# Kernel tuning notes

Measured on AMD Instinct MI355X. Metric: run time of the kernel, lower is better.

The kernel has to match this reference:

```python
import jax, jax.numpy as jnp
import numpy as np

B = 16
H_DIM = 512
N_HEADS = 8
HEAD_DIM = H_DIM // N_HEADS  # 64
EPS = 1e-5
DST_LENS = 256 + 16 * np.arange(B)  # ragged dst sizes, total 6016
SRC_LENS = 512 - 8 * np.arange(B)   # ragged src sizes, total 7232


def _pad_info(lens):
    # gather/scatter indices to move between flat ragged layout and [B, Lmax, D]
    lens = np.asarray(lens)
    off = np.concatenate([[0], np.cumsum(lens)[:-1]])
    gid = np.repeat(np.arange(len(lens)), lens)
    pos = np.arange(int(lens.sum())) - np.repeat(off, lens)
    Lmax = int(lens.max())
    mask = jnp.asarray(np.arange(Lmax)[None, :] < lens[:, None])
    return gid, pos, Lmax, mask


def _bn(x, g, b):
    # BatchNorm1d forward with batch statistics (training-mode normalization)
    m = x.mean(0)
    v = ((x - m) ** 2).mean(0)
    return (x - m) / jnp.sqrt(v + EPS) * g + b


def setup_inputs() -> dict:
    key = jax.random.key(0)
    ks = jax.random.split(key, 20)
    total_src = int(SRC_LENS.sum())
    total_dst = int(DST_LENS.sum())
    w = lambda k, shape: jax.random.normal(k, shape, jnp.float32) * 0.02
    return {
        "src_h": jax.random.normal(ks[0], (total_src, H_DIM), jnp.float32),
        "dst_h": jax.random.normal(ks[1], (total_dst, H_DIM), jnp.float32),
        "src_num_verts": jnp.asarray(SRC_LENS, jnp.int32),
        "dst_num_verts": jnp.asarray(DST_LENS, jnp.int32),
        "Wq": w(ks[2], (H_DIM, H_DIM)), "bq": w(ks[3], (H_DIM,)),
        "Wk": w(ks[4], (H_DIM, H_DIM)), "bk": w(ks[5], (H_DIM,)),
        "Wv": w(ks[6], (H_DIM, H_DIM)), "bv": w(ks[7], (H_DIM,)),
        "Wm": w(ks[8], (H_DIM, H_DIM)), "bm": w(ks[9], (H_DIM,)),
        "W1": w(ks[10], (H_DIM, 2 * H_DIM)), "b1": w(ks[11], (H_DIM,)),
        "g1": jnp.ones((H_DIM,), jnp.float32), "be1": jnp.zeros((H_DIM,), jnp.float32),
        "W2": w(ks[12], (H_DIM, H_DIM)), "b2": w(ks[13], (H_DIM,)),
        "g2": jnp.ones((H_DIM,), jnp.float32), "be2": jnp.zeros((H_DIM,), jnp.float32),
    }


def reference(src_h, dst_h, src_num_verts, dst_num_verts,
              Wq, bq, Wk, bk, Wv, bv, Wm, bm,
              W1, b1, g1, be1, W2, b2, g2, be2):
    s_lens = np.asarray(src_num_verts)
    d_lens = np.asarray(dst_num_verts)
    sg, sp, Ls, smask = _pad_info(s_lens)
    dg, dp, Ld, dmask = _pad_info(d_lens)

    # ragged -> padded [B, L, D]
    src_pad = jnp.zeros((B, Ls, H_DIM), src_h.dtype).at[sg, sp].set(src_h)
    dst_pad = jnp.zeros((B, Ld, H_DIM), dst_h.dtype).at[dg, dp].set(dst_h)

    # Conv1d(k=1) projections; channel c = d*num_heads + h -> reshape (head_dim, n_heads)
    q = (dst_pad @ Wq.T + bq).reshape(B, Ld, HEAD_DIM, N_HEADS)
    k = (src_pad @ Wk.T + bk).reshape(B, Ls, HEAD_DIM, N_HEADS)
    v = (src_pad @ Wv.T + bv).reshape(B, Ls, HEAD_DIM, N_HEADS)

    scores = jnp.einsum('bndh,bmdh->bhnm', q, k) / 8.0  # sqrt(head_dim)=8
    scores = jnp.where(smask[:, None, None, :], scores, -1e9)
    attn = jax.nn.softmax(scores, axis=-1)
    o = jnp.einsum('bhnm,bmdh->bndh', attn, v).reshape(B, Ld, H_DIM)
    o = o @ Wm.T + bm  # merge Conv1d(k=1)

    # padded -> ragged
    h_msg = o[dg, dp]  # [total_dst, h_dim]

    h = dst_h
    x = jnp.concatenate([h, h_msg], axis=-1)
    x = _bn(x @ W1.T + b1, g1, be1)
    x = jax.nn.relu(x)
    x = _bn(x @ W2.T + b2, g2, be2)
    return h + x
```

## Files before the change

kernel.cpp:

```cpp
#include <hip/hip_runtime.h>
#include <hip/hip_bf16.h>

#define H_DIM 512
#define N_HEADS 8
#define HEAD_DIM 64
#define NBATCH 16

typedef __attribute__((ext_vector_type(8))) short short8;
typedef __attribute__((ext_vector_type(4))) float floatx4;

typedef unsigned short us16;

#define SW3(r) ((((r) >> 1) & 3) | (((r) & 1) << 2))

__device__ inline unsigned short f2bf(float f) {
  unsigned int u = __float_as_uint(f);
  unsigned int r = (u + 0x7fffu + ((u >> 16) & 1u)) >> 16;
  return (unsigned short)r;
}

__device__ inline void gld16(const us16* g, us16* l) {
  __builtin_amdgcn_global_load_lds(
      (const __attribute__((address_space(1))) void*)g,
      (__attribute__((address_space(3))) void*)l, 16, 0, 0);
}

__global__ __launch_bounds__(256) void prep_all(
    const float* __restrict__ src_h, const float* __restrict__ dst_h,
    const float* __restrict__ Wq, const float* __restrict__ Wk,
    const float* __restrict__ Wv, const float* __restrict__ W1,
    const float* __restrict__ W2, const float* __restrict__ Wm,
    const float* __restrict__ b1, const float* __restrict__ bm,
    us16* __restrict__ src_bf, us16* __restrict__ dst_bf,
    us16* __restrict__ Wqb, us16* __restrict__ Wkv, us16* __restrict__ Wf,
    us16* __restrict__ W2b, float* __restrict__ b1p, float* __restrict__ st,
    int n_src, int n_dst) {
  __shared__ __align__(16) us16 As[64 * 48];
  __shared__ __align__(16) us16 Bs[64 * 48];
  const int blk = blockIdx.x;
  const int t = threadIdx.x;

  if (blk < 2048) {
    if (blk == 0) {
      float4 z = make_float4(0.f, 0.f, 0.f, 0.f);
      ((float4*)st)[t] = z;
      ((float4*)st)[t + 256] = z;
    }
    const float* srcs[7] = {src_h, dst_h, Wq, Wk, Wv, W1, W2};
    us16* dsts[7] = {src_bf, dst_bf, Wqb, Wkv, Wkv + 262144, Wf, W2b};
    int ns[7] = {n_src, n_dst, 262144, 262144, 262144, 262144, 262144};
    for (int rg = 0; rg < 7; ++rg) {
      const float* sp = srcs[rg];
      us16* dp = dsts[rg];
      const bool strided = (rg == 5);
      for (int i = (blk * 256 + t) * 4; i < ns[rg]; i += 2048 * 256 * 4) {
        int j = strided ? ((i >> 9) * 1024 + (i & 511)) : i;
        float4 v = *(const float4*)(sp + j);
        ushort4 o;
        o.x = f2bf(v.x); o.y = f2bf(v.y); o.z = f2bf(v.z); o.w = f2bf(v.w);
        *(ushort4*)(dp + j) = o;
      }
    }
  } else if (blk < 2112) {
    const int bx = (blk - 2048) & 7, byk = (blk - 2048) >> 3;
    const int w = t >> 6, lane = t & 63;
    const int lane15 = lane & 15, quad = lane >> 4;
    const int wm = w >> 1, wn = w & 1;
    const int bn_ = bx * 64, bk = byk * 64;
    floatx4 acc[2][2];
#pragma unroll
    for (int a = 0; a < 2; ++a)
#pragma unroll
      for (int c = 0; c < 2; ++c) acc[a][c] = (floatx4){0.f, 0.f, 0.f, 0.f};
    for (int j0 = 0; j0 < 512; j0 += 32) {
      {
        int n = t >> 2, jj0 = (t & 3) * 8;
        const float* rp = W1 + (size_t)(bn_ + n) * 1024 + 512 + j0 + jj0;
        float4 va = *(const float4*)(rp);
        float4 vb = *(const float4*)(rp + 4);
        ushort4 pa, pb;
        pa.x = f2bf(va.x); pa.y = f2bf(va.y); pa.z = f2bf(va.z); pa.w = f2bf(va.w);
        pb.x = f2bf(vb.x); pb.y = f2bf(vb.y); pb.z = f2bf(vb.z); pb.w = f2bf(vb.w);
        *(ushort4*)(As + n * 48 + jj0) = pa;
        *(ushort4*)(As + n * 48 + jj0 + 4) = pb;
      }
      {
        int jj = t >> 3, kc0 = (t & 7) * 8;
        const float* rp = Wm + (size_t)(j0 + jj) * 512 + bk + kc0;
        float4 va = *(const float4*)(rp);
        float4 vb = *(const float4*)(rp + 4);
        float vv[8] = {va.x, va.y, va.z, va.w, vb.x, vb.y, vb.z, vb.w};
#pragma unroll
        for (int e = 0; e < 8; ++e) Bs[(kc0 + e) * 48 + jj] = f2bf(vv[e]);
      }
      __syncthreads();
      short8 a_[2], b_[2];
#pragma unroll
      for (int mt = 0; mt < 2; ++mt)
        a_[mt] = *(const short8*)(As + (wm * 32 + mt * 16 + lane15) * 48 + quad * 8);
#pragma unroll
      for (int nt = 0; nt < 2; ++nt)
        b_[nt] = *(const short8*)(Bs + (wn * 32 + nt * 16 + lane15) * 48 + quad * 8);
#pragma unroll
      for (int mt = 0; mt < 2; ++mt)
#pragma unroll
        for (int nt = 0; nt < 2; ++nt)
          acc[mt][nt] = __builtin_amdgcn_mfma_f32_16x16x32_bf16(
              a_[mt], b_[nt], acc[mt][nt], 0, 0, 0);
      __syncthreads();
    }
#pragma unroll
    for (int mt = 0; mt < 2; ++mt) {
      int n0 = bn_ + wm * 32 + mt * 16 + quad * 4;
#pragma unroll
      for (int nt = 0; nt < 2; ++nt) {
        int k = bk + wn * 32 + nt * 16 + lane15;
#pragma unroll
        for (int r = 0; r < 4; ++r)
          Wf[(size_t)(n0 + r) * 1024 + 512 + k] = f2bf(acc[mt][nt][r]);
      }
    }
  } else {
    int n = (blk - 2112) * 256 + t;
    if (n < 512) {
      const float* rp = W1 + (size_t)n * 1024 + 512;
      float s = 0.f;
      for (int j = 0; j < 512; j += 4) {
        float4 a = *(const float4*)(rp + j);
        float4 c = *(const float4*)(bm + j);
        s += a.x * c.x + a.y * c.y + a.z * c.z + a.w * c.w;
      }
      b1p[n] = b1[n] + s;
    }
  }
}

__device__ inline void gemm_body(
    const us16* __restrict__ A1, const us16* __restrict__ A2,
    const us16* __restrict__ W,
    const float* __restrict__ bias0, const float* __restrict__ bias1,
    void* __restrict__ C0, void* __restrict__ C1, float* __restrict__ stats,
    int M, int N, int K, int mode, int bx, int by) {
  __shared__ __align__(16) us16 As[2 * 64 * 64];
  __shared__ __align__(16) us16 Bs[2 * 128 * 64];
  const int t = threadIdx.x, w = t >> 6, lane = t & 63;
  const int lane15 = lane & 15, quad = lane >> 4;
  const int bm = bx * 64, bn = by * 128;
  const int lrow = lane >> 3;
  const int sl = lane & 7;

  floatx4 acc[4][2];
#pragma unroll
  for (int a = 0; a < 4; ++a)
#pragma unroll
    for (int c = 0; c < 2; ++c) acc[a][c] = (floatx4){0.f, 0.f, 0.f, 0.f};

  const int nk = K >> 6;

#define ISSUE(i, b)                                                          \
  {                                                                          \
    int k0 = (i) << 6;                                                       \
    const us16* Ab = (k0 < 512) ? A1 : A2;                                   \
    int ka = k0 & 511;                                                       \
    _Pragma("unroll")                                                        \
    for (int p = 0; p < 2; ++p) {                                            \
      int rbase = p * 32 + w * 8;                                            \
      int row = rbase + lrow;                                                \
      int kg = sl ^ SW3(row);                                                \
      gld16(Ab + (size_t)(bm + row) * 512 + ka + kg * 8,                     \
            As + (b) * 4096 + rbase * 64);                                   \
    }                                                                        \
    _Pragma("unroll")                                                        \
    for (int p = 0; p < 4; ++p) {                                            \
      int rbase = p * 32 + w * 8;                                            \
      int row = rbase + lrow;                                                \
      int kg = sl ^ SW3(row);                                                \
      gld16(W + (size_t)(bn + row) * K + k0 + kg * 8,                        \
            Bs + (b) * 8192 + rbase * 64);                                   \
    }                                                                        \
  }

  ISSUE(0, 0);
  __syncthreads();
  for (int i = 0; i < nk; ++i) {
    const int cur = i & 1;
    if (i + 1 < nk) ISSUE(i + 1, cur ^ 1);
#pragma unroll
    for (int kh = 0; kh < 2; ++kh) {
      const int g = kh * 4 + quad;
      short8 a_[4], b_[2];
#pragma unroll
      for (int mt = 0; mt < 4; ++mt) {
        int r = mt * 16 + lane15;
        a_[mt] = *(const short8*)(As + cur * 4096 + r * 64 + (g ^ SW3(r)) * 8);
      }
#pragma unroll
      for (int nt = 0; nt < 2; ++nt) {
        int c = w * 32 + nt * 16 + lane15;
        b_[nt] = *(const short8*)(Bs + cur * 8192 + c * 64 + (g ^ SW3(c)) * 8);
      }
#pragma unroll
      for (int mt = 0; mt < 4; ++mt)
#pragma unroll
        for (int nt = 0; nt < 2; ++nt)
          acc[mt][nt] = __builtin_amdgcn_mfma_f32_16x16x32_bf16(
              a_[mt], b_[nt], acc[mt][nt], 0, 0, 0);
    }
    __syncthreads();
  }
#undef ISSUE

  if (mode == 0) {
#pragma unroll
    for (int nt = 0; nt < 2; ++nt) {
      int col = bn + w * 32 + nt * 16 + lane15;
      float bv = bias0[col];
      float s = 0.f, qq = 0.f;
#pragma unroll
      for (int mt = 0; mt < 4; ++mt) {
        int row0 = bm + mt * 16 + quad * 4;
#pragma unroll
        for (int r = 0; r < 4; ++r) {
          float val = acc[mt][nt][r] + bv;
          ((float*)C0)[(size_t)(row0 + r) * N + col] = val;
          s += val; qq = fmaf(val, val, qq);
        }
      }
      s += __shfl_xor(s, 16); s += __shfl_xor(s, 32);
      qq += __shfl_xor(qq, 16); qq += __shfl_xor(qq, 32);
      if (quad == 0) {
        atomicAdd(&stats[col], s);
        atomicAdd(&stats[512 + col], qq);
      }
    }
  } else if (mode == 1) {
#pragma unroll
    for (int nt = 0; nt < 2; ++nt) {
      int col = bn + w * 32 + nt * 16 + lane15;
      float bv = bias0[col];
      int hh = col & 7, dd = col >> 3;
#pragma unroll
      for (int mt = 0; mt < 4; ++mt) {
        int row0 = bm + mt * 16 + quad * 4;
#pragma unroll
        for (int r = 0; r < 4; ++r)
          ((us16*)C0)[((size_t)hh * M + row0 + r) * 64 + dd] = f2bf(acc[mt][nt][r] + bv);
      }
    }
  } else {
#pragma unroll
    for (int nt = 0; nt < 2; ++nt) {
      int col = bn + w * 32 + nt * 16 + lane15;
      if (col < 512) {
        float bv = bias0[col];
        int hh = col & 7, dd = col >> 3;
#pragma unroll
        for (int mt = 0; mt < 4; ++mt) {
          int row0 = bm + mt * 16 + quad * 4;
#pragma unroll
          for (int r = 0; r < 4; ++r)
            ((us16*)C0)[((size_t)hh * M + row0 + r) * 64 + dd] = f2bf(acc[mt][nt][r] + bv);
        }
      } else {
        int cv = col - 512;
        float bv = bias1[cv];
        int plane = (cv & 7) * 64 + (cv >> 3);
#pragma unroll
        for (int mt = 0; mt < 4; ++mt) {
          int row0 = bm + mt * 16 + quad * 4;
          ushort4 pk;
          pk.x = f2bf(acc[mt][nt][0] + bv);
          pk.y = f2bf(acc[mt][nt][1] + bv);
          pk.z = f2bf(acc[mt][nt][2] + bv);
          pk.w = f2bf(acc[mt][nt][3] + bv);
          *(ushort4*)((us16*)C1 + (size_t)plane * M + row0) = pk;
        }
      }
    }
  }
}

__global__ __launch_bounds__(256) void gemm_ffn(
    const us16* __restrict__ A1, const us16* __restrict__ A2,
    const us16* __restrict__ W,
    const float* __restrict__ bias0, void* __restrict__ C0,
    float* __restrict__ stats, int M, int K) {
  gemm_body(A1, A2, W, bias0, nullptr, C0, nullptr, stats, M, 512, K, 0,
            blockIdx.x >> 2, blockIdx.x & 3);
}

__global__ __launch_bounds__(256) void gemm_qkv(
    const us16* __restrict__ dst_bf, const us16* __restrict__ src_bf,
    const us16* __restrict__ Wqb, const us16* __restrict__ Wkv,
    const float* __restrict__ bq, const float* __restrict__ bk,
    const float* __restrict__ bv,
    us16* __restrict__ Qh, us16* __restrict__ Kh, us16* __restrict__ Vt,
    int Md, int Ms) {
  int i = blockIdx.x;
  int nq = (Md / 64) * 4;
  if (i < nq) {
    gemm_body(dst_bf, dst_bf, Wqb, bq, nullptr, Qh, nullptr, nullptr,
              Md, 512, 512, 1, i >> 2, i & 3);
  } else {
    int j = i - nq;
    gemm_body(src_bf, src_bf, Wkv, bk, bv, Kh, Vt, nullptr,
              Ms, 1024, 512, 4, j >> 3, j & 7);
  }
}

__global__ __launch_bounds__(256) void attn_v6(
    const us16* __restrict__ Qh, const us16* __restrict__ Kh,
    const us16* __restrict__ Vt, const int* __restrict__ dlens,
    const int* __restrict__ slens, us16* __restrict__ O,
    int Md, int Ms) {
  const int b = blockIdx.x, h = blockIdx.y, tile = blockIdx.z;
  int doff = 0, soff = 0;
  for (int i = 0; i < NBATCH; ++i)
    if (i < b) { doff += dlens[i]; soff += slens[i]; }
  const int dlen = dlens[b], slen = slens[b];
  if (tile * 64 >= dlen) return;

  __shared__ __align__(16) us16 Ks[64 * 64];
  __shared__ __align__(16) us16 Vts[64 * 64];
  __shared__ __align__(16) us16 Pw[4][16 * 72];

  const int t = threadIdx.x, wv = t >> 6, lane = t & 63;
  const int lane15 = lane & 15, quad = lane >> 4;
  const int i0w = tile * 64 + wv * 16;
  const bool active = i0w < dlen;

  const us16* Qp = Qh + ((size_t)h * Md + doff + (active ? i0w : 0)) * 64;
  const us16* Kp = Kh + ((size_t)h * Ms + soff) * 64;
  const us16* Vtp = Vt + ((size_t)h * 64) * Ms + soff;

  short8 af0 = *(const short8*)(Qp + (size_t)lane15 * 64 + quad * 8);
  short8 af1 = *(const short8*)(Qp + (size_t)lane15 * 64 + 32 + quad * 8);

  floatx4 oa[4];
#pragma unroll
  for (int nt = 0; nt < 4; ++nt) oa[nt] = (floatx4){0.f, 0.f, 0.f, 0.f};
  float m_r[4] = {-3.0e38f, -3.0e38f, -3.0e38f, -3.0e38f};
  float l_r[4] = {0.f, 0.f, 0.f, 0.f};

  for (int j0 = 0; j0 < slen; j0 += 64) {
#pragma unroll
    for (int p = 0; p < 2; ++p) {
      int row = wv * 16 + p * 8 + (lane >> 3);
      int sl = lane & 7;
      int kg = sl ^ SW3(row);
      gld16(Kp + (size_t)(j0 + row) * 64 + kg * 8, Ks + (wv * 16 + p * 8) * 64);
      gld16(Vtp + (size_t)row * Ms + j0 + kg * 8, Vts + (wv * 16 + p * 8) * 64);
    }
    __syncthreads();

    if (active) {
      floatx4 s[4];
#pragma unroll
      for (int jt = 0; jt < 4; ++jt) {
        int j = jt * 16 + lane15;
        short8 b0 = *(const short8*)(Ks + j * 64 + ((quad ^ SW3(j)) * 8));
        short8 b1 = *(const short8*)(Ks + j * 64 + (((4 + quad) ^ SW3(j)) * 8));
        floatx4 a = (floatx4){0.f, 0.f, 0.f, 0.f};
        a = __builtin_amdgcn_mfma_f32_16x16x32_bf16(af0, b0, a, 0, 0, 0);
        a = __builtin_amdgcn_mfma_f32_16x16x32_bf16(af1, b1, a, 0, 0, 0);
        s[jt] = a;
      }
      float mx[4] = {-3.0e38f, -3.0e38f, -3.0e38f, -3.0e38f};
#pragma unroll
      for (int jt = 0; jt < 4; ++jt) {
        bool valid = (j0 + jt * 16 + lane15) < slen;
#pragma unroll
        for (int r = 0; r < 4; ++r) {
          float v = valid ? s[jt][r] * 0.125f : -3.0e38f;
          s[jt][r] = v;
          mx[r] = fmaxf(mx[r], v);
        }
      }
#pragma unroll
      for (int r = 0; r < 4; ++r) {
        mx[r] = fmaxf(mx[r], __shfl_xor(mx[r], 1));
        mx[r] = fmaxf(mx[r], __shfl_xor(mx[r], 2));
        mx[r] = fmaxf(mx[r], __shfl_xor(mx[r], 4));
        mx[r] = fmaxf(mx[r], __shfl_xor(mx[r], 8));
      }
      float al[4], sum[4];
#pragma unroll
      for (int r = 0; r < 4; ++r) {
        float mn = fmaxf(m_r[r], mx[r]);
        al[r] = __expf(m_r[r] - mn);
        m_r[r] = mn;
        sum[r] = 0.f;
      }
#pragma unroll
      for (int jt = 0; jt < 4; ++jt)
#pragma unroll
        for (int r = 0; r < 4; ++r) {
          float e = __expf(s[jt][r] - m_r[r]);
          sum[r] += e;
          Pw[wv][(quad * 4 + r) * 72 + jt * 16 + lane15] = f2bf(e);
        }
#pragma unroll
      for (int r = 0; r < 4; ++r) {
        sum[r] += __shfl_xor(sum[r], 1);
        sum[r] += __shfl_xor(sum[r], 2);
        sum[r] += __shfl_xor(sum[r], 4);
        sum[r] += __shfl_xor(sum[r], 8);
        l_r[r] = l_r[r] * al[r] + sum[r];
      }
#pragma unroll
      for (int nt = 0; nt < 4; ++nt)
#pragma unroll
        for (int r = 0; r < 4; ++r) oa[nt][r] *= al[r];
      short8 pa0 = *(const short8*)(&Pw[wv][lane15 * 72 + quad * 8]);
      short8 pa1 = *(const short8*)(&Pw[wv][lane15 * 72 + 32 + quad * 8]);
#pragma unroll
      for (int nt = 0; nt < 4; ++nt) {
        int d = nt * 16 + lane15;
        short8 v0 = *(const short8*)(Vts + d * 64 + ((quad ^ SW3(d)) * 8));
        short8 v1 = *(const short8*)(Vts + d * 64 + (((4 + quad) ^ SW3(d)) * 8));
        oa[nt] = __builtin_amdgcn_mfma_f32_16x16x32_bf16(pa0, v0, oa[nt], 0, 0, 0);
        oa[nt] = __builtin_amdgcn_mfma_f32_16x16x32_bf16(pa1, v1, oa[nt], 0, 0, 0);
      }
    }
    __syncthreads();
  }

  if (active) {
    float linv[4];
#pragma unroll
    for (int r = 0; r < 4; ++r) linv[r] = 1.f / l_r[r];
#pragma unroll
    for (int r = 0; r < 4; ++r) {
      int i = quad * 4 + r;
      us16* orow = O + (size_t)(doff + i0w + i) * H_DIM + h;
#pragma unroll
      for (int nt = 0; nt < 4; ++nt) {
        int d = nt * 16 + lane15;
        orow[d * 8] = f2bf(oa[nt][r] * linv[r]);
      }
    }
  }
}

__global__ __launch_bounds__(256) void bn_apply(
    const float* __restrict__ X, const float* __restrict__ stats,
    const float* __restrict__ g, const float* __restrict__ be,
    const float* __restrict__ resid, void* __restrict__ Y,
    int M, float invM, int relu, int out_bf) {
  const size_t total = (size_t)M * H_DIM;
  for (size_t i = (size_t)blockIdx.x * 256 + threadIdx.x; i < total;
       i += (size_t)gridDim.x * 256) {
    int c = (int)(i & (H_DIM - 1));
    float mean = stats[c] * invM;
    float var = fmaf(-mean, mean, stats[H_DIM + c] * invM);
    float x = X[i];
    float y = (x - mean) * rsqrtf(var + 1e-5f) * g[c] + be[c];
    if (relu) y = fmaxf(y, 0.f);
    if (resid) y += resid[i];
    if (out_bf) ((us16*)Y)[i] = f2bf(y);
    else ((float*)Y)[i] = y;
  }
}

extern "C" void kernel_launch(void* const* d_in, const int* in_sizes, int n_in,
                              void* d_out, int out_size, void* d_ws, size_t ws_size,
                              hipStream_t stream) {
  const float* src_h = (const float*)d_in[0];
  const float* dst_h = (const float*)d_in[1];
  const int* s_lens  = (const int*)d_in[2];
  const int* d_lens  = (const int*)d_in[3];
  const float* Wq = (const float*)d_in[4];  const float* bq = (const float*)d_in[5];
  const float* Wk = (const float*)d_in[6];  const float* bk = (const float*)d_in[7];
  const float* Wv = (const float*)d_in[8];  const float* bv = (const float*)d_in[9];
  const float* Wm = (const float*)d_in[10]; const float* bm = (const float*)d_in[11];
  const float* W1 = (const float*)d_in[12]; const float* b1 = (const float*)d_in[13];
  const float* g1 = (const float*)d_in[14]; const float* be1 = (const float*)d_in[15];
  const float* W2 = (const float*)d_in[16]; const float* b2 = (const float*)d_in[17];
  const float* g2 = (const float*)d_in[18]; const float* be2 = (const float*)d_in[19];

  const int total_src = in_sizes[0] / H_DIM;
  const int total_dst = in_sizes[1] / H_DIM;

  char* ws = (char*)d_ws;
  us16* src_bf = (us16*)(ws + 0);
  us16* dst_bf = (us16*)(ws + 7405568);
  us16* wbf    = (us16*)(ws + 13565952);
  float* b1p   = (float*)(ws + 16711680);
  us16* Qh     = (us16*)(ws + 17235968);
  us16* Kh     = (us16*)(ws + 23396352);
  us16* Vt     = (us16*)(ws + 30801920);
  us16* Ob     = (us16*)(ws + 38207488);
  us16* X1bf   = (us16*)(ws + 44367872);
  float* st    = (float*)(ws + 50528256);
  float* X1    = (float*)(ws + 17235968);
  float* X2    = (float*)(ws + 30801920);
  float* st1 = st, *st2 = st + 1024;

  us16* Wqb = wbf;
  us16* Wkv = wbf + 262144;
  us16* Wf  = wbf + 786432;
  us16* W2b = wbf + 1310720;

  const int mbd = total_dst / 64;
  const int mbs = total_src / 64;
  const dim3 blk256(256);

  prep_all<<<dim3(2114), blk256, 0, stream>>>(
      src_h, dst_h, Wq, Wk, Wv, W1, W2, Wm, b1, bm,
      src_bf, dst_bf, Wqb, Wkv, Wf, W2b, b1p, st,
      total_src * H_DIM, total_dst * H_DIM);

  gemm_qkv<<<dim3(mbd * 4 + mbs * 8), blk256, 0, stream>>>(
      dst_bf, src_bf, Wqb, Wkv, bq, bk, bv, Qh, Kh, Vt, total_dst, total_src);

  attn_v6<<<dim3(NBATCH, N_HEADS, 8), blk256, 0, stream>>>(
      Qh, Kh, Vt, d_lens, s_lens, Ob, total_dst, total_src);

  gemm_ffn<<<dim3(mbd * 4), blk256, 0, stream>>>(
      dst_bf, Ob, Wf, b1p, X1, st1, total_dst, 1024);

  bn_apply<<<dim3(512), blk256, 0, stream>>>(X1, st1, g1, be1, nullptr, X1bf,
                                             total_dst, 1.f / (float)total_dst, 1, 1);

  gemm_ffn<<<dim3(mbd * 4), blk256, 0, stream>>>(
      X1bf, X1bf, W2b, b2, X2, st2, total_dst, 512);

  bn_apply<<<dim3(512), blk256, 0, stream>>>(X2, st2, g2, be2, dst_h, d_out,
                                             total_dst, 1.f / (float)total_dst, 0, 0);
}
```

Baseline: 258.2 us.

## Deepen GEMM to triple-buffered and attention to double-buffered async pipelines

The GEMM main loop moves from a double buffer to a three-stage LDS ring. Loads are issued two K-steps ahead, and a vmcnt wait plus a raw barrier replace the two __syncthreads per step. The attention kernel double-buffers its K/V tiles and prefetches the chunk two steps ahead, so global loads overlap the MFMA and softmax work. Both GEMM launches also remap block indices with an 8-way stride swizzle to change scheduling and cache locality. The cost is more LDS per block, which may lower occupancy, and the hand-counted vmcnt values are fragile if the number of loads per stage changes.

```diff
diff --git a/kernel.cpp b/kernel.cpp
--- a/kernel.cpp
+++ b/kernel.cpp
@@ -141,8 +141,8 @@
     const float* __restrict__ bias0, const float* __restrict__ bias1,
     void* __restrict__ C0, void* __restrict__ C1, float* __restrict__ stats,
     int M, int N, int K, int mode, int bx, int by) {
-  __shared__ __align__(16) us16 As[2 * 64 * 64];
-  __shared__ __align__(16) us16 Bs[2 * 128 * 64];
+  __shared__ __align__(16) us16 As[3 * 64 * 64];
+  __shared__ __align__(16) us16 Bs[3 * 128 * 64];
   const int t = threadIdx.x, w = t >> 6, lane = t & 63;
   const int lane15 = lane & 15, quad = lane >> 4;
   const int bm = bx * 64, bn = by * 128;
@@ -181,10 +181,21 @@
   }
 
   ISSUE(0, 0);
-  __syncthreads();
+  if (nk > 1) ISSUE(1, 1);
+  int cur = 0;
   for (int i = 0; i < nk; ++i) {
-    const int cur = i & 1;
-    if (i + 1 < nk) ISSUE(i + 1, cur ^ 1);
+    if (i + 1 < nk) {
+      asm volatile("s_waitcnt vmcnt(6)" ::: "memory");
+    } else {
+      asm volatile("s_waitcnt vmcnt(0)" ::: "memory");
+    }
+    __builtin_amdgcn_s_barrier();
+    asm volatile("" ::: "memory");
+    if (i + 2 < nk) {
+      int nb = cur + 2;
+      if (nb >= 3) nb -= 3;
+      ISSUE(i + 2, nb);
+    }
 #pragma unroll
     for (int kh = 0; kh < 2; ++kh) {
       const int g = kh * 4 + quad;
@@ -206,7 +217,7 @@
           acc[mt][nt] = __builtin_amdgcn_mfma_f32_16x16x32_bf16(
               a_[mt], b_[nt], acc[mt][nt], 0, 0, 0);
     }
-    __syncthreads();
+    cur = (cur == 2) ? 0 : cur + 1;
   }
 #undef ISSUE
 
@@ -285,8 +296,10 @@
     const us16* __restrict__ W,
     const float* __restrict__ bias0, void* __restrict__ C0,
     float* __restrict__ stats, int M, int K) {
+  int b = blockIdx.x;
+  int i = (b & 7) * ((int)gridDim.x >> 3) + (b >> 3);
   gemm_body(A1, A2, W, bias0, nullptr, C0, nullptr, stats, M, 512, K, 0,
-            blockIdx.x >> 2, blockIdx.x & 3);
+            i >> 2, i & 3);
 }
 
 __global__ __launch_bounds__(256) void gemm_qkv(
@@ -296,7 +309,8 @@
     const float* __restrict__ bv,
     us16* __restrict__ Qh, us16* __restrict__ Kh, us16* __restrict__ Vt,
     int Md, int Ms) {
-  int i = blockIdx.x;
+  int b = blockIdx.x;
+  int i = (b & 7) * ((int)gridDim.x >> 3) + (b >> 3);
   int nq = (Md / 64) * 4;
   if (i < nq) {
     gemm_body(dst_bf, dst_bf, Wqb, bq, nullptr, Qh, nullptr, nullptr,
@@ -320,8 +334,8 @@
   const int dlen = dlens[b], slen = slens[b];
   if (tile * 64 >= dlen) return;
 
-  __shared__ __align__(16) us16 Ks[64 * 64];
-  __shared__ __align__(16) us16 Vts[64 * 64];
+  __shared__ __align__(16) us16 Ks[2 * 64 * 64];
+  __shared__ __align__(16) us16 Vts[2 * 64 * 64];
   __shared__ __align__(16) us16 Pw[4][16 * 72];
 
   const int t = threadIdx.x, wv = t >> 6, lane = t & 63;
@@ -342,24 +356,43 @@
   float m_r[4] = {-3.0e38f, -3.0e38f, -3.0e38f, -3.0e38f};
   float l_r[4] = {0.f, 0.f, 0.f, 0.f};
 
-  for (int j0 = 0; j0 < slen; j0 += 64) {
-#pragma unroll
-    for (int p = 0; p < 2; ++p) {
-      int row = wv * 16 + p * 8 + (lane >> 3);
-      int sl = lane & 7;
-      int kg = sl ^ SW3(row);
-      gld16(Kp + (size_t)(j0 + row) * 64 + kg * 8, Ks + (wv * 16 + p * 8) * 64);
-      gld16(Vtp + (size_t)row * Ms + j0 + kg * 8, Vts + (wv * 16 + p * 8) * 64);
-    }
-    __syncthreads();
+  const int nc = (slen + 63) >> 6;
+
+#define KVST(c, bu)                                                       \
+  {                                                                       \
+    int jb = (c) << 6;                                                    \
+    _Pragma("unroll")                                                     \
+    for (int p = 0; p < 2; ++p) {                                         \
+      int row = wv * 16 + p * 8 + (lane >> 3);                            \
+      int slt = lane & 7;                                                 \
+      int kg = slt ^ SW3(row);                                            \
+      gld16(Kp + (size_t)(jb + row) * 64 + kg * 8,                        \
+            Ks + (bu) * 4096 + (wv * 16 + p * 8) * 64);                   \
+      gld16(Vtp + (size_t)row * Ms + jb + kg * 8,                         \
+            Vts + (bu) * 4096 + (wv * 16 + p * 8) * 64);                  \
+    }                                                                     \
+  }
+
+  KVST(0, 0);
+  if (nc > 1) KVST(1, 1);
+  for (int c = 0; c < nc; ++c) {
+    const int cur = c & 1;
+    if (c + 1 < nc) {
+      asm volatile("s_waitcnt vmcnt(4)" ::: "memory");
+    } else {
+      asm volatile("s_waitcnt vmcnt(0)" ::: "memory");
+    }
+    __builtin_amdgcn_s_barrier();
+    asm volatile("" ::: "memory");
 
     if (active) {
+      const int j0 = c << 6;
       floatx4 s[4];
 #pragma unroll
       for (int jt = 0; jt < 4; ++jt) {
         int j = jt * 16 + lane15;
-        short8 b0 = *(const short8*)(Ks + j * 64 + ((quad ^ SW3(j)) * 8));
-        short8 b1 = *(const short8*)(Ks + j * 64 + (((4 + quad) ^ SW3(j)) * 8));
+        short8 b0 = *(const short8*)(Ks + cur * 4096 + j * 64 + ((quad ^ SW3(j)) * 8));
+        short8 b1 = *(const short8*)(Ks + cur * 4096 + j * 64 + (((4 + quad) ^ SW3(j)) * 8));
         floatx4 a = (floatx4){0.f, 0.f, 0.f, 0.f};
         a = __builtin_amdgcn_mfma_f32_16x16x32_bf16(af0, b0, a, 0, 0, 0);
         a = __builtin_amdgcn_mfma_f32_16x16x32_bf16(af1, b1, a, 0, 0, 0);
@@ -416,14 +449,19 @@
 #pragma unroll
       for (int nt = 0; nt < 4; ++nt) {
         int d = nt * 16 + lane15;
-        short8 v0 = *(const short8*)(Vts + d * 64 + ((quad ^ SW3(d)) * 8));
-        short8 v1 = *(const short8*)(Vts + d * 64 + (((4 + quad) ^ SW3(d)) * 8));
+        short8 v0 = *(const short8*)(Vts + cur * 4096 + d * 64 + ((quad ^ SW3(d)) * 8));
+        short8 v1 = *(const short8*)(Vts + cur * 4096 + d * 64 + (((4 + quad) ^ SW3(d)) * 8));
         oa[nt] = __builtin_amdgcn_mfma_f32_16x16x32_bf16(pa0, v0, oa[nt], 0, 0, 0);
         oa[nt] = __builtin_amdgcn_mfma_f32_16x16x32_bf16(pa1, v1, oa[nt], 0, 0, 0);
       }
     }
-    __syncthreads();
-  }
+
+    asm volatile("" ::: "memory");
+    __builtin_amdgcn_s_barrier();
+    asm volatile("" ::: "memory");
+    if (c + 2 < nc) KVST(c + 2, cur);
+  }
+#undef KVST
 
   if (active) {
     float linv[4];
```

New measurement: 258.3 us. No clear change (+0.0%).
